# Performance work log

Hardware: AMD Instinct MI355X
Metric: run time of the kernel (lower is better)

## Reference

```python
import jax, jax.numpy as jnp
import numpy as np

N_NODES = 100000
N_EDGES = 1600000
IN_C, HID_C, OUT_C = 26, 128, 64
BN_EPS = 1e-5
WEIGHT_TABLE = jnp.array([0.7,0.9,0.7,0.9,0.3,0.7,0.3,0.9,0.3,0.3,0.9,0.7,0.1,
                          0.9,0.5,0.9,0.5,0.5,0.1,0.3,0.7,0.9,0.9,0.9,0.9,0.9],
                         dtype=jnp.float32)


def setup_inputs() -> dict:
    key = jax.random.key(0)
    ks = jax.random.split(key, 20)
    d = {}
    d['h'] = jax.random.normal(ks[0], (N_NODES, IN_C), dtype=jnp.float32)
    d['src'] = jax.random.randint(ks[1], (N_EDGES,), 0, N_NODES, dtype=jnp.int32)
    d['dst'] = jax.random.randint(ks[2], (N_EDGES,), 0, N_NODES, dtype=jnp.int32)
    # GraphConv weights (Glorot-ish scale)
    d['w0'] = jax.random.normal(ks[3], (IN_C, HID_C), dtype=jnp.float32) * (1.0 / np.sqrt(IN_C))
    d['b0'] = jnp.zeros((HID_C,), jnp.float32)
    d['w1'] = jax.random.normal(ks[4], (HID_C, HID_C), dtype=jnp.float32) * (1.0 / np.sqrt(HID_C))
    d['b1'] = jnp.zeros((HID_C,), jnp.float32)
    d['w2'] = jax.random.normal(ks[5], (HID_C, HID_C), dtype=jnp.float32) * (1.0 / np.sqrt(HID_C))
    d['b2'] = jnp.zeros((HID_C,), jnp.float32)
    # BatchNorm affine params
    for i in range(3):
        d[f'g{i}'] = jnp.ones((HID_C,), jnp.float32)
        d[f'bt{i}'] = jnp.zeros((HID_C,), jnp.float32)
    d['wfc'] = jax.random.normal(ks[6], (HID_C, OUT_C), dtype=jnp.float32) * (1.0 / np.sqrt(HID_C))
    d['bfc'] = jnp.zeros((OUT_C,), jnp.float32)
    return d


def _degree_norms(src, dst):
    ones = jnp.ones((N_EDGES,), jnp.float32)
    deg_out = jax.ops.segment_sum(ones, src, num_segments=N_NODES)
    deg_in = jax.ops.segment_sum(ones, dst, num_segments=N_NODES)
    norm_src = jnp.clip(deg_out, 1.0, None) ** -0.5  # [N]
    norm_dst = jnp.clip(deg_in, 1.0, None) ** -0.5   # [N]
    return norm_src[:, None], norm_dst[:, None]


def _graph_conv(h, W, b, src, dst, norm_src, norm_dst):
    # DGL GraphConv, norm='both': D_dst^{-1/2} A^T D_src^{-1/2} X W + b
    y = (h * norm_src) @ W                                   # [N, out]
    agg = jax.ops.segment_sum(y[src], dst, num_segments=N_NODES)
    return agg * norm_dst + b


def _batch_norm(x, gamma, beta):
    mu = jnp.mean(x, axis=0)
    var = jnp.mean((x - mu) ** 2, axis=0)
    return (x - mu) * jax.lax.rsqrt(var + BN_EPS) * gamma + beta


def reference(h, src, dst, w0, b0, w1, b1, w2, b2,
              g0, bt0, g1, bt1, g2, bt2, wfc, bfc):
    node_cats = jnp.argmax(h, axis=1)
    node_weights = WEIGHT_TABLE[node_cats][:, None]  # [N,1]
    norm_src, norm_dst = _degree_norms(src, dst)
    x = h
    for W, b, g, bt in ((w0, b0, g0, bt0), (w1, b1, g1, bt1), (w2, b2, g2, bt2)):
        x = _graph_conv(x, W, b, src, dst, norm_src, norm_dst)
        x = _batch_norm(x, g, bt)
        x = jax.nn.relu(x)
    out = x @ wfc + bfc
    return out, node_weights
```

## Files before the change

### kernel.cpp

```cpp
#include <hip/hip_runtime.h>

#define NN 100000
#define NE 1600000
#define BN_EPS 1e-5f
#define CSHIFT 9
#define NBC ((NN + 511) >> CSHIFT)
#define CAPC 10240
#define EPB1 4096
#define NBLK1 ((NE + EPB1 - 1)/EPB1)
#define NTILES ((NN + 63)/64)
#define GGRID 521
#define NPAGE 64

typedef short bf16x8 __attribute__((ext_vector_type(8)));
typedef float f32x4  __attribute__((ext_vector_type(4)));

__constant__ float c_wtab[26] = {0.7f,0.9f,0.7f,0.9f,0.3f,0.7f,0.3f,0.9f,0.3f,0.3f,0.9f,0.7f,0.1f,
                                 0.9f,0.5f,0.9f,0.5f,0.5f,0.1f,0.3f,0.7f,0.9f,0.9f,0.9f,0.9f,0.9f};

__device__ __forceinline__ unsigned f2bf(float f){
    unsigned u = __float_as_uint(f);
    return (u + 0x7fffu + ((u >> 16) & 1u)) >> 16;
}
__device__ __forceinline__ float bflo(unsigned v){ return __uint_as_float(v << 16); }
__device__ __forceinline__ float bfhi(unsigned v){ return __uint_as_float(v & 0xffff0000u); }

__global__ void k_prepw(const float* __restrict__ w0, const float* __restrict__ w1,
                        const float* __restrict__ w2, const float* __restrict__ wfc,
                        unsigned short* __restrict__ wt){
    int i = blockIdx.x*256 + threadIdx.x;
    if (i < 4096){
        int c = i >> 5, k = i & 31;
        float v = (k < 26) ? w0[k*128 + c] : 0.f;
        wt[i] = (unsigned short)f2bf(v);
    } else if (i < 20480){
        int j = i - 4096; int c = j >> 7, k = j & 127;
        wt[i] = (unsigned short)f2bf(w1[k*128 + c]);
    } else if (i < 36864){
        int j = i - 20480; int c = j >> 7, k = j & 127;
        wt[i] = (unsigned short)f2bf(w2[k*128 + c]);
    } else if (i < 45056){
        int j = i - 36864; int c = j >> 7, k = j & 127;
        wt[i] = (unsigned short)f2bf(wfc[k*64 + c]);
    }
}

__global__ void k_init(unsigned* __restrict__ gcurD, unsigned* __restrict__ gcurS){
    int i = blockIdx.x*256 + threadIdx.x;
    if (i < NBC){ gcurD[i] = (unsigned)i*CAPC; gcurS[i] = (unsigned)i*CAPC; }
}

__global__ __launch_bounds__(512) void k_radix1(const int* __restrict__ src,
                                                const int* __restrict__ dst,
                                                unsigned* __restrict__ gcurD,
                                                unsigned* __restrict__ gcurS,
                                                unsigned* __restrict__ pairs,
                                                unsigned short* __restrict__ tok){
    __shared__ unsigned hD[NBC], hS[NBC];
    int tid = threadIdx.x;
    for (int i = tid; i < NBC; i += 512){ hD[i] = 0u; hS[i] = 0u; }
    __syncthreads();
    int base = blockIdx.x*EPB1;
    int n = NE - base; if (n > EPB1) n = EPB1;
    for (int k = tid; k < n; k += 512){
        atomicAdd(&hD[(unsigned)dst[base+k] >> CSHIFT], 1u);
        atomicAdd(&hS[(unsigned)src[base+k] >> CSHIFT], 1u);
    }
    __syncthreads();
    for (int i = tid; i < NBC; i += 512){
        unsigned c = hD[i];
        hD[i] = c ? atomicAdd(&gcurD[i], c) : 0u;
        c = hS[i];
        hS[i] = c ? atomicAdd(&gcurS[i], c) : 0u;
    }
    __syncthreads();
    for (int k = tid; k < n; k += 512){
        int d = dst[base+k], s = src[base+k];
        unsigned bb = (unsigned)d >> CSHIFT;
        unsigned p = atomicAdd(&hD[bb], 1u);
        if (p < (bb+1)*CAPC)
            pairs[p] = ((unsigned)(d & 511) << 17) | (unsigned)s;
        bb = (unsigned)s >> CSHIFT;
        p = atomicAdd(&hS[bb], 1u);
        if (p < (bb+1)*CAPC)
            tok[p] = (unsigned short)(s & 511);
    }
}

__global__ __launch_bounds__(1024) void k_radix2(const unsigned* __restrict__ gcurD,
                                                 const unsigned* __restrict__ gcurS,
                                                 const unsigned* __restrict__ pairs,
                                                 const unsigned short* __restrict__ tok,
                                                 int* __restrict__ csr,
                                                 unsigned* __restrict__ offs,
                                                 unsigned* __restrict__ degi,
                                                 unsigned* __restrict__ dego){
    __shared__ unsigned cnt[512], cur[512], scnt[512];
    int b = blockIdx.x, tid = threadIdx.x;
    if (tid < 512){ cnt[tid] = 0u; scnt[tid] = 0u; }
    __syncthreads();
    unsigned baseC = (unsigned)b*CAPC;
    unsigned nD = gcurD[b] - baseC; if (nD > CAPC) nD = CAPC;
    unsigned nS = gcurS[b] - baseC; if (nS > CAPC) nS = CAPC;
    for (unsigned i = tid; i < nD; i += 1024)
        atomicAdd(&cnt[pairs[baseC + i] >> 17], 1u);
    for (unsigned i = tid; i < nS; i += 1024)
        atomicAdd(&scnt[tok[baseC + i]], 1u);
    __syncthreads();
    if (tid < 512) cur[tid] = cnt[tid];
    __syncthreads();
    for (int o = 1; o < 512; o <<= 1){
        unsigned x = 0;
        if (tid < 512 && tid >= o) x = cur[tid - o];
        __syncthreads();
        if (tid < 512) cur[tid] += x;
        __syncthreads();
    }
    if (tid < 512){
        unsigned ex = cur[tid] - cnt[tid];
        int node = (b << CSHIFT) + tid;
        if (node < NN){
            offs[node] = baseC + ex;
            degi[node] = cnt[tid];
            dego[node] = scnt[tid];
        }
        cur[tid] = ex;
    }
    __syncthreads();
    for (unsigned i = tid; i < nD; i += 1024){
        unsigned pr = pairs[baseC + i];
        unsigned p = atomicAdd(&cur[pr >> 17], 1u);
        csr[baseC + p] = (int)(pr & 0x1FFFFu);
    }
}

__global__ void k_node(const float* __restrict__ h, const unsigned* __restrict__ dego,
                       const unsigned* __restrict__ degi, float* __restrict__ nsrc,
                       float* __restrict__ ndst, float* __restrict__ outw,
                       unsigned* __restrict__ xn0){
    int i = blockIdx.x*blockDim.x + threadIdx.x;
    if (i < NN){
        float d0 = (float)dego[i]; d0 = d0 < 1.f ? 1.f : d0;
        float d1 = (float)degi[i]; d1 = d1 < 1.f ? 1.f : d1;
        float ns = rsqrtf(d0);
        nsrc[i] = ns;
        ndst[i] = rsqrtf(d1);
        float row[26];
        #pragma unroll
        for (int c = 0; c < 26; ++c) row[c] = h[(size_t)i*26 + c];
        float best = row[0]; int bi = 0;
        #pragma unroll
        for (int c = 1; c < 26; ++c){ if (row[c] > best){ best = row[c]; bi = c; } }
        outw[i] = c_wtab[bi];
        #pragma unroll
        for (int d = 0; d < 13; ++d)
            xn0[(size_t)i*16 + d] = f2bf(row[2*d]*ns) | (f2bf(row[2*d+1]*ns) << 16);
        #pragma unroll
        for (int d = 13; d < 16; ++d) xn0[(size_t)i*16 + d] = 0u;
    }
}

__global__ __launch_bounds__(64) void k_agg0(const uint4* __restrict__ xn,
                                             const unsigned* __restrict__ offs,
                                             const unsigned* __restrict__ degi,
                                             const int* __restrict__ csr,
                                             uint4* __restrict__ agg){
    int node = blockIdx.x;
    int lane = threadIdx.x;
    int g = lane >> 2, q = lane & 3;
    unsigned beg = offs[node], end = beg + degi[node];
    float a[8];
    #pragma unroll
    for (int j = 0; j < 8; ++j) a[j] = 0.f;
    for (unsigned e = beg + (unsigned)g; e < end; e += 16){
        uint4 v = xn[(size_t)csr[e]*4 + q];
        a[0] += bflo(v.x); a[1] += bfhi(v.x);
        a[2] += bflo(v.y); a[3] += bfhi(v.y);
        a[4] += bflo(v.z); a[5] += bfhi(v.z);
        a[6] += bflo(v.w); a[7] += bfhi(v.w);
    }
    #pragma unroll
    for (int j = 0; j < 8; ++j){
        a[j] += __shfl_xor(a[j], 4);
        a[j] += __shfl_xor(a[j], 8);
        a[j] += __shfl_xor(a[j], 16);
        a[j] += __shfl_xor(a[j], 32);
    }
    if (g == 0){
        uint4 o;
        o.x = f2bf(a[0]) | (f2bf(a[1]) << 16);
        o.y = f2bf(a[2]) | (f2bf(a[3]) << 16);
        o.z = f2bf(a[4]) | (f2bf(a[5]) << 16);
        o.w = f2bf(a[6]) | (f2bf(a[7]) << 16);
        agg[(size_t)node*4 + q] = o;
    }
}

__global__ __launch_bounds__(64) void k_agg_bf(const uint4* __restrict__ xn,
                                               const unsigned* __restrict__ offs,
                                               const unsigned* __restrict__ degi,
                                               const int* __restrict__ csr,
                                               uint4* __restrict__ agg){
    int node = blockIdx.x;
    int lane = threadIdx.x;
    int g = lane >> 4, q = lane & 15;
    unsigned beg = offs[node], end = beg + degi[node];
    float a[8];
    #pragma unroll
    for (int j = 0; j < 8; ++j) a[j] = 0.f;
    unsigned e = beg + (unsigned)g;
    for (; e + 12 < end; e += 16){
        int s0 = csr[e], s1 = csr[e+4], s2 = csr[e+8], s3 = csr[e+12];
        uint4 v0 = xn[(size_t)s0*16 + q];
        uint4 v1 = xn[(size_t)s1*16 + q];
        uint4 v2 = xn[(size_t)s2*16 + q];
        uint4 v3 = xn[(size_t)s3*16 + q];
        a[0] += bflo(v0.x) + bflo(v1.x) + bflo(v2.x) + bflo(v3.x);
        a[1] += bfhi(v0.x) + bfhi(v1.x) + bfhi(v2.x) + bfhi(v3.x);
        a[2] += bflo(v0.y) + bflo(v1.y) + bflo(v2.y) + bflo(v3.y);
        a[3] += bfhi(v0.y) + bfhi(v1.y) + bfhi(v2.y) + bfhi(v3.y);
        a[4] += bflo(v0.z) + bflo(v1.z) + bflo(v2.z) + bflo(v3.z);
        a[5] += bfhi(v0.z) + bfhi(v1.z) + bfhi(v2.z) + bfhi(v3.z);
        a[6] += bflo(v0.w) + bflo(v1.w) + bflo(v2.w) + bflo(v3.w);
        a[7] += bfhi(v0.w) + bfhi(v1.w) + bfhi(v2.w) + bfhi(v3.w);
    }
    for (; e < end; e += 4){
        uint4 v = xn[(size_t)csr[e]*16 + q];
        a[0] += bflo(v.x); a[1] += bfhi(v.x);
        a[2] += bflo(v.y); a[3] += bfhi(v.y);
        a[4] += bflo(v.z); a[5] += bfhi(v.z);
        a[6] += bflo(v.w); a[7] += bfhi(v.w);
    }
    #pragma unroll
    for (int j = 0; j < 8; ++j){
        a[j] += __shfl_xor(a[j], 16);
        a[j] += __shfl_xor(a[j], 32);
    }
    if (g == 0){
        uint4 o;
        o.x = f2bf(a[0]) | (f2bf(a[1]) << 16);
        o.y = f2bf(a[2]) | (f2bf(a[3]) << 16);
        o.z = f2bf(a[4]) | (f2bf(a[5]) << 16);
        o.w = f2bf(a[6]) | (f2bf(a[7]) << 16);
        agg[(size_t)node*16 + q] = o;
    }
}

template<int CIN, int COUT, bool STATS, bool NDST, bool F32OUT>
__global__ __launch_bounds__(256) void k_gemm_mfma(const unsigned short* __restrict__ A,
                                                   const unsigned short* __restrict__ Bt,
                                                   const float* __restrict__ bias,
                                                   const float* __restrict__ ndst,
                                                   void* __restrict__ Zv,
                                                   float* __restrict__ part){
    constexpr int KD4 = CIN/8;
    constexpr int NT = COUT/16;
    __shared__ char sA[64*CIN*2];
    __shared__ char sB[COUT*CIN*2];
    __shared__ float sS[2][COUT];
    float* Zf = (float*)Zv;
    unsigned short* Zh = (unsigned short*)Zv;
    const int tid = threadIdx.x;
    const int w = tid >> 6, lane = tid & 63;
    const int lrow = lane & 15, kg = lane >> 4;

    const uint4* B4 = (const uint4*)Bt;
    for (int i = tid; i < COUT*KD4; i += 256){
        int cc = i/KD4, c4 = i - cc*KD4;
        *(uint4*)(sB + ((cc*CIN*2 + c4*16) ^ ((cc&7)<<4))) = B4[i];
    }
    if (STATS){
        for (int i = tid; i < 2*COUT; i += 256) (&sS[0][0])[i] = 0.f;
    }

    float cs[NT], cq[NT];
    #pragma unroll
    for (int n = 0; n < NT; ++n){ cs[n] = 0.f; cq[n] = 0.f; }

    const uint4* A4 = (const uint4*)A;
    const uint4 z4 = make_uint4(0,0,0,0);
    for (int t = blockIdx.x; t < NTILES; t += GGRID){
        const int row0 = t*64;
        for (int i = tid; i < 64*KD4; i += 256){
            int r = i/KD4, c4 = i - r*KD4;
            int gr = row0 + r;
            uint4 v = (gr < NN) ? A4[(size_t)gr*KD4 + c4] : z4;
            *(uint4*)(sA + ((r*CIN*2 + c4*16) ^ ((r&7)<<4))) = v;
        }
        __syncthreads();
        f32x4 acc[NT];
        #pragma unroll
        for (int n = 0; n < NT; ++n) acc[n] = (f32x4){0.f,0.f,0.f,0.f};
        const int arow = w*16 + lrow;
        #pragma unroll
        for (int kk = 0; kk < CIN/32; ++kk){
            const int kb = kk*64 + kg*16;
            bf16x8 af = *(const bf16x8*)(sA + ((arow*CIN*2 + kb) ^ ((arow&7)<<4)));
            #pragma unroll
            for (int n = 0; n < NT; ++n){
                int bc = n*16 + lrow;
                bf16x8 bv = *(const bf16x8*)(sB + ((bc*CIN*2 + kb) ^ ((bc&7)<<4)));
                acc[n] = __builtin_amdgcn_mfma_f32_16x16x32_bf16(af, bv, acc[n], 0, 0, 0);
            }
        }
        int grow[4]; float nm[4]; bool val[4];
        #pragma unroll
        for (int j = 0; j < 4; ++j){
            grow[j] = row0 + w*16 + kg*4 + j;
            val[j]  = grow[j] < NN;
            nm[j]   = (NDST && val[j]) ? ndst[grow[j]] : 1.f;
        }
        #pragma unroll
        for (int n = 0; n < NT; ++n){
            int gcol = n*16 + lrow;
            float bv = bias[gcol];
            #pragma unroll
            for (int j = 0; j < 4; ++j){
                float z = acc[n][j]*nm[j] + bv;
                if (val[j]){
                    if (F32OUT) Zf[(size_t)grow[j]*COUT + gcol] = z;
                    else        Zh[(size_t)grow[j]*COUT + gcol] = (unsigned short)f2bf(z);
                    if (STATS){ cs[n] += z; cq[n] += z*z; }
                }
            }
        }
        __syncthreads();
    }
    if (STATS){
        #pragma unroll
        for (int n = 0; n < NT; ++n){
            float s = cs[n], q = cq[n];
            s += __shfl_xor(s, 16); s += __shfl_xor(s, 32);
            q += __shfl_xor(q, 16); q += __shfl_xor(q, 32);
            if (kg == 0){
                atomicAdd(&sS[0][n*16 + lrow], s);
                atomicAdd(&sS[1][n*16 + lrow], q);
            }
        }
        __syncthreads();
        float* pg = part + (size_t)(blockIdx.x & (NPAGE-1))*2*COUT;
        for (int i = tid; i < 2*COUT; i += 256)
            atomicAdd(&pg[i], (&sS[0][0])[i]);
    }
}

__global__ void k_bnfin(const float* __restrict__ part, float* __restrict__ stats,
                        const float* __restrict__ g, const float* __restrict__ bt){
    int c = threadIdx.x;
    float s = 0.f, q = 0.f;
    #pragma unroll 8
    for (int p = 0; p < NPAGE; ++p){
        s += part[p*256 + c];
        q += part[p*256 + 128 + c];
    }
    float mu  = s / (float)NN;
    float var = q / (float)NN - mu*mu;
    if (var < 0.f) var = 0.f;
    float sc = g[c] * rsqrtf(var + BN_EPS);
    stats[256 + c] = sc;
    stats[384 + c] = bt[c] - mu*sc;
}

__global__ void k_bnapply_bf(const unsigned* __restrict__ Xb, const float* __restrict__ stats,
                             const float* __restrict__ nsrc, unsigned* __restrict__ out){
    int idx = blockIdx.x*blockDim.x + threadIdx.x;
    if (idx < NN*64){
        int d = idx & 63;
        int node = idx >> 6;
        int c0 = d << 1;
        unsigned v = Xb[idx];
        float v0 = bflo(v)*stats[256 + c0]     + stats[384 + c0];
        float v1 = bfhi(v)*stats[256 + c0 + 1] + stats[384 + c0 + 1];
        float ns = nsrc ? nsrc[node] : 1.f;
        v0 = v0 > 0.f ? v0*ns : 0.f;
        v1 = v1 > 0.f ? v1*ns : 0.f;
        out[idx] = f2bf(v0) | (f2bf(v1) << 16);
    }
}

extern "C" void kernel_launch(void* const* d_in, const int* in_sizes, int n_in,
                              void* d_out, int out_size, void* d_ws, size_t ws_size,
                              hipStream_t stream) {
    const float* h   = (const float*)d_in[0];
    const int*   src = (const int*)d_in[1];
    const int*   dst = (const int*)d_in[2];
    const float* w0  = (const float*)d_in[3];
    const float* b0  = (const float*)d_in[4];
    const float* w1  = (const float*)d_in[5];
    const float* b1  = (const float*)d_in[6];
    const float* w2  = (const float*)d_in[7];
    const float* b2  = (const float*)d_in[8];
    const float* g0  = (const float*)d_in[9];
    const float* bt0 = (const float*)d_in[10];
    const float* g1  = (const float*)d_in[11];
    const float* bt1 = (const float*)d_in[12];
    const float* g2  = (const float*)d_in[13];
    const float* bt2 = (const float*)d_in[14];
    const float* wfc = (const float*)d_in[15];
    const float* bfc = (const float*)d_in[16];

    float* out   = (float*)d_out;
    float* out_w = out + (size_t)NN*64;

    char* ws = (char*)d_ws;
    size_t off = 0;
    auto alloc = [&](size_t b){ size_t p = off; off += (b + 255) & ~(size_t)255; return ws + p; };

    unsigned*       dego    = (unsigned*)alloc((size_t)NN*4);
    unsigned*       degi    = (unsigned*)alloc((size_t)NN*4);
    float*          nsrc    = (float*)   alloc((size_t)NN*4);
    float*          ndst    = (float*)   alloc((size_t)NN*4);
    unsigned*       offsets = (unsigned*)alloc((size_t)NN*4);
    unsigned*       gcurD   = (unsigned*)alloc((size_t)NBC*4);
    unsigned*       gcurS   = (unsigned*)alloc((size_t)NBC*4);
    float*          stats   = (float*)   alloc(3*512*4);
    float*          spart   = (float*)   alloc(3*(size_t)NPAGE*256*4);
    unsigned short* wt      = (unsigned short*)alloc(45056*2);
    int*            csr     = (int*)     alloc((size_t)NBC*CAPC*4);
    unsigned*       xn0     = (unsigned*)alloc((size_t)NN*16*4);
    unsigned short* bufA    = (unsigned short*)alloc((size_t)NN*128*2);
    float*          bufB    = (float*)   alloc((size_t)NN*128*4);
    unsigned*       bufC    = (unsigned*)alloc((size_t)NN*64*4);
    (void)ws_size; (void)in_sizes; (void)n_in; (void)out_size;

    unsigned*       pairs = (unsigned*)bufB;
    unsigned short* tok   = (unsigned short*)((char*)bufB + (size_t)NBC*CAPC*4);
    uint4*          aggB  = (uint4*)bufB;

    hipMemsetAsync(spart, 0, 3*(size_t)NPAGE*256*4, stream);

    k_prepw<<<176, 256, 0, stream>>>(w0, w1, w2, wfc, wt);
    k_init<<<1, 256, 0, stream>>>(gcurD, gcurS);
    k_radix1<<<NBLK1, 512, 0, stream>>>(src, dst, gcurD, gcurS, pairs, tok);
    k_radix2<<<NBC, 1024, 0, stream>>>(gcurD, gcurS, pairs, tok, csr, offsets, degi, dego);
    k_node<<<(NN + 255)/256, 256, 0, stream>>>(h, dego, degi, nsrc, ndst, out_w, xn0);

    k_agg0<<<NN, 64, 0, stream>>>((const uint4*)xn0, offsets, degi, csr, aggB);
    k_gemm_mfma<32,128,true,true,false><<<GGRID, 256, 0, stream>>>((const unsigned short*)aggB, wt, b0,
                                                                   ndst, bufA, spart + 0*NPAGE*256);
    k_bnfin<<<1, 128, 0, stream>>>(spart + 0*NPAGE*256, stats + 0*512, g0, bt0);
    k_bnapply_bf<<<(NN*64 + 255)/256, 256, 0, stream>>>((unsigned*)bufA, stats + 0*512, nsrc, bufC);

    k_agg_bf<<<NN, 64, 0, stream>>>((const uint4*)bufC, offsets, degi, csr, aggB);
    k_gemm_mfma<128,128,true,true,false><<<GGRID, 256, 0, stream>>>((const unsigned short*)aggB, wt + 4096,
                                                                    b1, ndst, bufA, spart + 1*NPAGE*256);
    k_bnfin<<<1, 128, 0, stream>>>(spart + 1*NPAGE*256, stats + 1*512, g1, bt1);
    k_bnapply_bf<<<(NN*64 + 255)/256, 256, 0, stream>>>((unsigned*)bufA, stats + 1*512, nsrc, bufC);

    k_agg_bf<<<NN, 64, 0, stream>>>((const uint4*)bufC, offsets, degi, csr, aggB);
    k_gemm_mfma<128,128,true,true,false><<<GGRID, 256, 0, stream>>>((const unsigned short*)aggB, wt + 20480,
                                                                    b2, ndst, bufA, spart + 2*NPAGE*256);
    k_bnfin<<<1, 128, 0, stream>>>(spart + 2*NPAGE*256, stats + 2*512, g2, bt2);
    k_bnapply_bf<<<(NN*64 + 255)/256, 256, 0, stream>>>((unsigned*)bufA, stats + 2*512, nullptr, bufC);

    k_gemm_mfma<128,64,false,false,true><<<GGRID, 256, 0, stream>>>((unsigned short*)bufC, wt + 36864, bfc,
                                                                    nullptr, out, nullptr);
}
```

Before: 370.5 us.

## Store hidden features in 16-channel slices and aggregate per slice

Node features are now stored as 8 slices of 16 channels each, so one slice holds 32 bytes per node. The aggregation kernel gives each block one slice for 8 nodes, and each pair of lanes gathers one edge's 32-byte fragment. BN-apply writes this sliced layout and the GEMMs read it through a new SLICED template flag. The aim is a smaller working set per gather for better cache locality, at the cost of 8x more reads of the CSR index and smaller, less coalesced memory transactions per edge.

```diff
diff --git a/kernel.cpp b/kernel.cpp
--- a/kernel.cpp
+++ b/kernel.cpp
@@ -11,6 +11,7 @@
 #define NTILES ((NN + 63)/64)
 #define GGRID 521
 #define NPAGE 64
+#define SLNN ((size_t)NN*2)
 
 typedef short bf16x8 __attribute__((ext_vector_type(8)));
 typedef float f32x4  __attribute__((ext_vector_type(4)));
@@ -196,36 +197,27 @@
     }
 }
 
-__global__ __launch_bounds__(64) void k_agg_bf(const uint4* __restrict__ xn,
-                                               const unsigned* __restrict__ offs,
-                                               const unsigned* __restrict__ degi,
-                                               const int* __restrict__ csr,
-                                               uint4* __restrict__ agg){
-    int node = blockIdx.x;
-    int lane = threadIdx.x;
-    int g = lane >> 4, q = lane & 15;
+__global__ __launch_bounds__(256) void k_agg_bf(const uint4* __restrict__ xnS,
+                                                const unsigned* __restrict__ offs,
+                                                const unsigned* __restrict__ degi,
+                                                const int* __restrict__ csr,
+                                                uint4* __restrict__ aggS){
+    const int slice = blockIdx.x & 7;
+    const int ng = blockIdx.x >> 3;
+    const int tid = threadIdx.x;
+    const int w = tid >> 6, lane = tid & 63;
+    const int half = lane >> 5;
+    const int node = ng*8 + w*2 + half;
+    const int el = (lane & 31) >> 1;
+    const int q = lane & 1;
+    const uint4* base = xnS + (size_t)slice*SLNN;
     unsigned beg = offs[node], end = beg + degi[node];
     float a[8];
     #pragma unroll
     for (int j = 0; j < 8; ++j) a[j] = 0.f;
-    unsigned e = beg + (unsigned)g;
-    for (; e + 12 < end; e += 16){
-        int s0 = csr[e], s1 = csr[e+4], s2 = csr[e+8], s3 = csr[e+12];
-        uint4 v0 = xn[(size_t)s0*16 + q];
-        uint4 v1 = xn[(size_t)s1*16 + q];
-        uint4 v2 = xn[(size_t)s2*16 + q];
-        uint4 v3 = xn[(size_t)s3*16 + q];
-        a[0] += bflo(v0.x) + bflo(v1.x) + bflo(v2.x) + bflo(v3.x);
-        a[1] += bfhi(v0.x) + bfhi(v1.x) + bfhi(v2.x) + bfhi(v3.x);
-        a[2] += bflo(v0.y) + bflo(v1.y) + bflo(v2.y) + bflo(v3.y);
-        a[3] += bfhi(v0.y) + bfhi(v1.y) + bfhi(v2.y) + bfhi(v3.y);
-        a[4] += bflo(v0.z) + bflo(v1.z) + bflo(v2.z) + bflo(v3.z);
-        a[5] += bfhi(v0.z) + bfhi(v1.z) + bfhi(v2.z) + bfhi(v3.z);
-        a[6] += bflo(v0.w) + bflo(v1.w) + bflo(v2.w) + bflo(v3.w);
-        a[7] += bfhi(v0.w) + bfhi(v1.w) + bfhi(v2.w) + bfhi(v3.w);
-    }
-    for (; e < end; e += 4){
-        uint4 v = xn[(size_t)csr[e]*16 + q];
+    for (unsigned e = beg + (unsigned)el; e < end; e += 16){
+        int s = csr[e];
+        uint4 v = base[(size_t)s*2 + q];
         a[0] += bflo(v.x); a[1] += bfhi(v.x);
         a[2] += bflo(v.y); a[3] += bfhi(v.y);
         a[4] += bflo(v.z); a[5] += bfhi(v.z);
@@ -233,20 +225,22 @@
     }
     #pragma unroll
     for (int j = 0; j < 8; ++j){
+        a[j] += __shfl_xor(a[j], 2);
+        a[j] += __shfl_xor(a[j], 4);
+        a[j] += __shfl_xor(a[j], 8);
         a[j] += __shfl_xor(a[j], 16);
-        a[j] += __shfl_xor(a[j], 32);
-    }
-    if (g == 0){
+    }
+    if (el == 0){
         uint4 o;
         o.x = f2bf(a[0]) | (f2bf(a[1]) << 16);
         o.y = f2bf(a[2]) | (f2bf(a[3]) << 16);
         o.z = f2bf(a[4]) | (f2bf(a[5]) << 16);
         o.w = f2bf(a[6]) | (f2bf(a[7]) << 16);
-        agg[(size_t)node*16 + q] = o;
-    }
-}
-
-template<int CIN, int COUT, bool STATS, bool NDST, bool F32OUT>
+        aggS[(size_t)slice*SLNN + (size_t)node*2 + q] = o;
+    }
+}
+
+template<int CIN, int COUT, bool STATS, bool NDST, bool F32OUT, bool SLICED>
 __global__ __launch_bounds__(256) void k_gemm_mfma(const unsigned short* __restrict__ A,
                                                    const unsigned short* __restrict__ Bt,
                                                    const float* __restrict__ bias,
@@ -284,7 +278,11 @@
         for (int i = tid; i < 64*KD4; i += 256){
             int r = i/KD4, c4 = i - r*KD4;
             int gr = row0 + r;
-            uint4 v = (gr < NN) ? A4[(size_t)gr*KD4 + c4] : z4;
+            uint4 v;
+            if (gr < NN){
+                if (SLICED) v = A4[(size_t)(c4 >> 1)*SLNN + (size_t)gr*2 + (c4 & 1)];
+                else        v = A4[(size_t)gr*KD4 + c4];
+            } else v = z4;
             *(uint4*)(sA + ((r*CIN*2 + c4*16) ^ ((r&7)<<4))) = v;
         }
         __syncthreads();
@@ -362,7 +360,7 @@
 }
 
 __global__ void k_bnapply_bf(const unsigned* __restrict__ Xb, const float* __restrict__ stats,
-                             const float* __restrict__ nsrc, unsigned* __restrict__ out){
+                             const float* __restrict__ nsrc, unsigned* __restrict__ outS){
     int idx = blockIdx.x*blockDim.x + threadIdx.x;
     if (idx < NN*64){
         int d = idx & 63;
@@ -374,7 +372,8 @@
         float ns = nsrc ? nsrc[node] : 1.f;
         v0 = v0 > 0.f ? v0*ns : 0.f;
         v1 = v1 > 0.f ? v1*ns : 0.f;
-        out[idx] = f2bf(v0) | (f2bf(v1) << 16);
+        int slice = d >> 3, dd = d & 7;
+        outS[(size_t)slice*NN*8 + (size_t)node*8 + dd] = f2bf(v0) | (f2bf(v1) << 16);
     }
 }
 
@@ -436,23 +435,23 @@
     k_node<<<(NN + 255)/256, 256, 0, stream>>>(h, dego, degi, nsrc, ndst, out_w, xn0);
 
     k_agg0<<<NN, 64, 0, stream>>>((const uint4*)xn0, offsets, degi, csr, aggB);
-    k_gemm_mfma<32,128,true,true,false><<<GGRID, 256, 0, stream>>>((const unsigned short*)aggB, wt, b0,
-                                                                   ndst, bufA, spart + 0*NPAGE*256);
+    k_gemm_mfma<32,128,true,true,false,false><<<GGRID, 256, 0, stream>>>((const unsigned short*)aggB, wt, b0,
+                                                                         ndst, bufA, spart + 0*NPAGE*256);
     k_bnfin<<<1, 128, 0, stream>>>(spart + 0*NPAGE*256, stats + 0*512, g0, bt0);
     k_bnapply_bf<<<(NN*64 + 255)/256, 256, 0, stream>>>((unsigned*)bufA, stats + 0*512, nsrc, bufC);
 
-    k_agg_bf<<<NN, 64, 0, stream>>>((const uint4*)bufC, offsets, degi, csr, aggB);
-    k_gemm_mfma<128,128,true,true,false><<<GGRID, 256, 0, stream>>>((const unsigned short*)aggB, wt + 4096,
-                                                                    b1, ndst, bufA, spart + 1*NPAGE*256);
+    k_agg_bf<<<NN, 256, 0, stream>>>((const uint4*)bufC, offsets, degi, csr, aggB);
+    k_gemm_mfma<128,128,true,true,false,true><<<GGRID, 256, 0, stream>>>((const unsigned short*)aggB, wt + 4096,
+                                                                         b1, ndst, bufA, spart + 1*NPAGE*256);
     k_bnfin<<<1, 128, 0, stream>>>(spart + 1*NPAGE*256, stats + 1*512, g1, bt1);
     k_bnapply_bf<<<(NN*64 + 255)/256, 256, 0, stream>>>((unsigned*)bufA, stats + 1*512, nsrc, bufC);
 
-    k_agg_bf<<<NN, 64, 0, stream>>>((const uint4*)bufC, offsets, degi, csr, aggB);
-    k_gemm_mfma<128,128,true,true,false><<<GGRID, 256, 0, stream>>>((const unsigned short*)aggB, wt + 20480,
-                                                                    b2, ndst, bufA, spart + 2*NPAGE*256);
+    k_agg_bf<<<NN, 256, 0, stream>>>((const uint4*)bufC, offsets, degi, csr, aggB);
+    k_gemm_mfma<128,128,true,true,false,true><<<GGRID, 256, 0, stream>>>((const unsigned short*)aggB, wt + 20480,
+                                                                         b2, ndst, bufA, spart + 2*NPAGE*256);
     k_bnfin<<<1, 128, 0, stream>>>(spart + 2*NPAGE*256, stats + 2*512, g2, bt2);
     k_bnapply_bf<<<(NN*64 + 255)/256, 256, 0, stream>>>((unsigned*)bufA, stats + 2*512, nullptr, bufC);
 
-    k_gemm_mfma<128,64,false,false,true><<<GGRID, 256, 0, stream>>>((unsigned short*)bufC, wt + 36864, bfc,
-                                                                    nullptr, out, nullptr);
-}
+    k_gemm_mfma<128,64,false,false,true,true><<<GGRID, 256, 0, stream>>>((unsigned short*)bufC, wt + 36864, bfc,
+                                                                         nullptr, out, nullptr);
+}
```

Measured after the change: 523.9 us. 41.4% more time.

## Fuse BN-apply/ReLU into aggregation and final GEMM; merge prep and node kernels

Applied to the files above, without the earlier changes.

Removes the three standalone BatchNorm-apply kernels. The scale/shift, ReLU and source-norm are now applied on the fly inside the gather-aggregation (per edge) and inside the final GEMM's A-tile load. Folds k_init into weight prep and the per-node norm/argmax kernel into radix2, which cuts launches and the dego buffer. Each gathered row now costs extra FMAs plus a per-edge nsrc load, trading compute for one fewer full read/write pass per layer.

```diff
diff --git a/kernel.cpp b/kernel.cpp
--- a/kernel.cpp
+++ b/kernel.cpp
@@ -25,9 +25,10 @@
 __device__ __forceinline__ float bflo(unsigned v){ return __uint_as_float(v << 16); }
 __device__ __forceinline__ float bfhi(unsigned v){ return __uint_as_float(v & 0xffff0000u); }
 
-__global__ void k_prepw(const float* __restrict__ w0, const float* __restrict__ w1,
-                        const float* __restrict__ w2, const float* __restrict__ wfc,
-                        unsigned short* __restrict__ wt){
+__global__ void k_prep(const float* __restrict__ w0, const float* __restrict__ w1,
+                       const float* __restrict__ w2, const float* __restrict__ wfc,
+                       unsigned short* __restrict__ wt,
+                       unsigned* __restrict__ gcurD, unsigned* __restrict__ gcurS){
     int i = blockIdx.x*256 + threadIdx.x;
     if (i < 4096){
         int c = i >> 5, k = i & 31;
@@ -43,10 +44,6 @@
         int j = i - 36864; int c = j >> 7, k = j & 127;
         wt[i] = (unsigned short)f2bf(wfc[k*64 + c]);
     }
-}
-
-__global__ void k_init(unsigned* __restrict__ gcurD, unsigned* __restrict__ gcurS){
-    int i = blockIdx.x*256 + threadIdx.x;
     if (i < NBC){ gcurD[i] = (unsigned)i*CAPC; gcurS[i] = (unsigned)i*CAPC; }
 }
 
@@ -87,14 +84,18 @@
     }
 }
 
-__global__ __launch_bounds__(1024) void k_radix2(const unsigned* __restrict__ gcurD,
-                                                 const unsigned* __restrict__ gcurS,
-                                                 const unsigned* __restrict__ pairs,
-                                                 const unsigned short* __restrict__ tok,
-                                                 int* __restrict__ csr,
-                                                 unsigned* __restrict__ offs,
-                                                 unsigned* __restrict__ degi,
-                                                 unsigned* __restrict__ dego){
+__global__ __launch_bounds__(1024) void k_radix2n(const unsigned* __restrict__ gcurD,
+                                                  const unsigned* __restrict__ gcurS,
+                                                  const unsigned* __restrict__ pairs,
+                                                  const unsigned short* __restrict__ tok,
+                                                  const float* __restrict__ h,
+                                                  int* __restrict__ csr,
+                                                  unsigned* __restrict__ offs,
+                                                  unsigned* __restrict__ degi,
+                                                  float* __restrict__ nsrc,
+                                                  float* __restrict__ ndst,
+                                                  float* __restrict__ outw,
+                                                  unsigned* __restrict__ xn0){
     __shared__ unsigned cnt[512], cur[512], scnt[512];
     int b = blockIdx.x, tid = threadIdx.x;
     if (tid < 512){ cnt[tid] = 0u; scnt[tid] = 0u; }
@@ -122,7 +123,6 @@
         if (node < NN){
             offs[node] = baseC + ex;
             degi[node] = cnt[tid];
-            dego[node] = scnt[tid];
         }
         cur[tid] = ex;
     }
@@ -132,31 +132,27 @@
         unsigned p = atomicAdd(&cur[pr >> 17], 1u);
         csr[baseC + p] = (int)(pr & 0x1FFFFu);
     }
-}
-
-__global__ void k_node(const float* __restrict__ h, const unsigned* __restrict__ dego,
-                       const unsigned* __restrict__ degi, float* __restrict__ nsrc,
-                       float* __restrict__ ndst, float* __restrict__ outw,
-                       unsigned* __restrict__ xn0){
-    int i = blockIdx.x*blockDim.x + threadIdx.x;
-    if (i < NN){
-        float d0 = (float)dego[i]; d0 = d0 < 1.f ? 1.f : d0;
-        float d1 = (float)degi[i]; d1 = d1 < 1.f ? 1.f : d1;
-        float ns = rsqrtf(d0);
-        nsrc[i] = ns;
-        ndst[i] = rsqrtf(d1);
-        float row[26];
-        #pragma unroll
-        for (int c = 0; c < 26; ++c) row[c] = h[(size_t)i*26 + c];
-        float best = row[0]; int bi = 0;
-        #pragma unroll
-        for (int c = 1; c < 26; ++c){ if (row[c] > best){ best = row[c]; bi = c; } }
-        outw[i] = c_wtab[bi];
-        #pragma unroll
-        for (int d = 0; d < 13; ++d)
-            xn0[(size_t)i*16 + d] = f2bf(row[2*d]*ns) | (f2bf(row[2*d+1]*ns) << 16);
-        #pragma unroll
-        for (int d = 13; d < 16; ++d) xn0[(size_t)i*16 + d] = 0u;
+    if (tid < 512){
+        int node = (b << CSHIFT) + tid;
+        if (node < NN){
+            float d0 = (float)scnt[tid]; d0 = d0 < 1.f ? 1.f : d0;
+            float d1 = (float)cnt[tid];  d1 = d1 < 1.f ? 1.f : d1;
+            float ns = rsqrtf(d0);
+            nsrc[node] = ns;
+            ndst[node] = rsqrtf(d1);
+            float row[26];
+            #pragma unroll
+            for (int c = 0; c < 26; ++c) row[c] = h[(size_t)node*26 + c];
+            float best = row[0]; int bi = 0;
+            #pragma unroll
+            for (int c = 1; c < 26; ++c){ if (row[c] > best){ best = row[c]; bi = c; } }
+            outw[node] = c_wtab[bi];
+            #pragma unroll
+            for (int d = 0; d < 13; ++d)
+                xn0[(size_t)node*16 + d] = f2bf(row[2*d]*ns) | (f2bf(row[2*d+1]*ns) << 16);
+            #pragma unroll
+            for (int d = 13; d < 16; ++d) xn0[(size_t)node*16 + d] = 0u;
+        }
     }
 }
 
@@ -196,7 +192,9 @@
     }
 }
 
-__global__ __launch_bounds__(64) void k_agg_bf(const uint4* __restrict__ xn,
+__global__ __launch_bounds__(64) void k_agg_bn(const uint4* __restrict__ zt,
+                                               const float* __restrict__ st,
+                                               const float* __restrict__ nsrc,
                                                const unsigned* __restrict__ offs,
                                                const unsigned* __restrict__ degi,
                                                const int* __restrict__ csr,
@@ -204,6 +202,12 @@
     int node = blockIdx.x;
     int lane = threadIdx.x;
     int g = lane >> 4, q = lane & 15;
+    float sc8[8], sh8[8];
+    #pragma unroll
+    for (int j = 0; j < 8; ++j){
+        sc8[j] = st[256 + q*8 + j];
+        sh8[j] = st[384 + q*8 + j];
+    }
     unsigned beg = offs[node], end = beg + degi[node];
     float a[8];
     #pragma unroll
@@ -211,25 +215,39 @@
     unsigned e = beg + (unsigned)g;
     for (; e + 12 < end; e += 16){
         int s0 = csr[e], s1 = csr[e+4], s2 = csr[e+8], s3 = csr[e+12];
-        uint4 v0 = xn[(size_t)s0*16 + q];
-        uint4 v1 = xn[(size_t)s1*16 + q];
-        uint4 v2 = xn[(size_t)s2*16 + q];
-        uint4 v3 = xn[(size_t)s3*16 + q];
-        a[0] += bflo(v0.x) + bflo(v1.x) + bflo(v2.x) + bflo(v3.x);
-        a[1] += bfhi(v0.x) + bfhi(v1.x) + bfhi(v2.x) + bfhi(v3.x);
-        a[2] += bflo(v0.y) + bflo(v1.y) + bflo(v2.y) + bflo(v3.y);
-        a[3] += bfhi(v0.y) + bfhi(v1.y) + bfhi(v2.y) + bfhi(v3.y);
-        a[4] += bflo(v0.z) + bflo(v1.z) + bflo(v2.z) + bflo(v3.z);
-        a[5] += bfhi(v0.z) + bfhi(v1.z) + bfhi(v2.z) + bfhi(v3.z);
-        a[6] += bflo(v0.w) + bflo(v1.w) + bflo(v2.w) + bflo(v3.w);
-        a[7] += bfhi(v0.w) + bfhi(v1.w) + bfhi(v2.w) + bfhi(v3.w);
+        float n0 = nsrc[s0], n1 = nsrc[s1], n2 = nsrc[s2], n3 = nsrc[s3];
+        uint4 v0 = zt[(size_t)s0*16 + q];
+        uint4 v1 = zt[(size_t)s1*16 + q];
+        uint4 v2 = zt[(size_t)s2*16 + q];
+        uint4 v3 = zt[(size_t)s3*16 + q];
+        #pragma unroll
+        for (int k = 0; k < 4; ++k){
+            uint4 v = (k==0)?v0:(k==1)?v1:(k==2)?v2:v3;
+            float nn = (k==0)?n0:(k==1)?n1:(k==2)?n2:n3;
+            float t;
+            t = fmaf(bflo(v.x), sc8[0], sh8[0]); t = t > 0.f ? t : 0.f; a[0] = fmaf(t, nn, a[0]);
+            t = fmaf(bfhi(v.x), sc8[1], sh8[1]); t = t > 0.f ? t : 0.f; a[1] = fmaf(t, nn, a[1]);
+            t = fmaf(bflo(v.y), sc8[2], sh8[2]); t = t > 0.f ? t : 0.f; a[2] = fmaf(t, nn, a[2]);
+            t = fmaf(bfhi(v.y), sc8[3], sh8[3]); t = t > 0.f ? t : 0.f; a[3] = fmaf(t, nn, a[3]);
+            t = fmaf(bflo(v.z), sc8[4], sh8[4]); t = t > 0.f ? t : 0.f; a[4] = fmaf(t, nn, a[4]);
+            t = fmaf(bfhi(v.z), sc8[5], sh8[5]); t = t > 0.f ? t : 0.f; a[5] = fmaf(t, nn, a[5]);
+            t = fmaf(bflo(v.w), sc8[6], sh8[6]); t = t > 0.f ? t : 0.f; a[6] = fmaf(t, nn, a[6]);
+            t = fmaf(bfhi(v.w), sc8[7], sh8[7]); t = t > 0.f ? t : 0.f; a[7] = fmaf(t, nn, a[7]);
+        }
     }
     for (; e < end; e += 4){
-        uint4 v = xn[(size_t)csr[e]*16 + q];
-        a[0] += bflo(v.x); a[1] += bfhi(v.x);
-        a[2] += bflo(v.y); a[3] += bfhi(v.y);
-        a[4] += bflo(v.z); a[5] += bfhi(v.z);
-        a[6] += bflo(v.w); a[7] += bfhi(v.w);
+        int s = csr[e];
+        float nn = nsrc[s];
+        uint4 v = zt[(size_t)s*16 + q];
+        float t;
+        t = fmaf(bflo(v.x), sc8[0], sh8[0]); t = t > 0.f ? t : 0.f; a[0] = fmaf(t, nn, a[0]);
+        t = fmaf(bfhi(v.x), sc8[1], sh8[1]); t = t > 0.f ? t : 0.f; a[1] = fmaf(t, nn, a[1]);
+        t = fmaf(bflo(v.y), sc8[2], sh8[2]); t = t > 0.f ? t : 0.f; a[2] = fmaf(t, nn, a[2]);
+        t = fmaf(bfhi(v.y), sc8[3], sh8[3]); t = t > 0.f ? t : 0.f; a[3] = fmaf(t, nn, a[3]);
+        t = fmaf(bflo(v.z), sc8[4], sh8[4]); t = t > 0.f ? t : 0.f; a[4] = fmaf(t, nn, a[4]);
+        t = fmaf(bfhi(v.z), sc8[5], sh8[5]); t = t > 0.f ? t : 0.f; a[5] = fmaf(t, nn, a[5]);
+        t = fmaf(bflo(v.w), sc8[6], sh8[6]); t = t > 0.f ? t : 0.f; a[6] = fmaf(t, nn, a[6]);
+        t = fmaf(bfhi(v.w), sc8[7], sh8[7]); t = t > 0.f ? t : 0.f; a[7] = fmaf(t, nn, a[7]);
     }
     #pragma unroll
     for (int j = 0; j < 8; ++j){
@@ -246,13 +264,14 @@
     }
 }
 
-template<int CIN, int COUT, bool STATS, bool NDST, bool F32OUT>
+template<int CIN, int COUT, bool STATS, bool NDST, bool F32OUT, bool BNIN>
 __global__ __launch_bounds__(256) void k_gemm_mfma(const unsigned short* __restrict__ A,
                                                    const unsigned short* __restrict__ Bt,
                                                    const float* __restrict__ bias,
                                                    const float* __restrict__ ndst,
                                                    void* __restrict__ Zv,
-                                                   float* __restrict__ part){
+                                                   float* __restrict__ part,
+                                                   const float* __restrict__ bn){
     constexpr int KD4 = CIN/8;
     constexpr int NT = COUT/16;
     __shared__ char sA[64*CIN*2];
@@ -285,6 +304,19 @@
             int r = i/KD4, c4 = i - r*KD4;
             int gr = row0 + r;
             uint4 v = (gr < NN) ? A4[(size_t)gr*KD4 + c4] : z4;
+            if (BNIN && gr < NN){
+                int ch = c4*8;
+                unsigned dw[4] = {v.x, v.y, v.z, v.w};
+                #pragma unroll
+                for (int k = 0; k < 4; ++k){
+                    float f0 = fmaf(bflo(dw[k]), bn[256 + ch + 2*k],     bn[384 + ch + 2*k]);
+                    float f1 = fmaf(bfhi(dw[k]), bn[256 + ch + 2*k + 1], bn[384 + ch + 2*k + 1]);
+                    f0 = f0 > 0.f ? f0 : 0.f;
+                    f1 = f1 > 0.f ? f1 : 0.f;
+                    dw[k] = f2bf(f0) | (f2bf(f1) << 16);
+                }
+                v = make_uint4(dw[0], dw[1], dw[2], dw[3]);
+            }
             *(uint4*)(sA + ((r*CIN*2 + c4*16) ^ ((r&7)<<4))) = v;
         }
         __syncthreads();
@@ -359,23 +391,6 @@
     float sc = g[c] * rsqrtf(var + BN_EPS);
     stats[256 + c] = sc;
     stats[384 + c] = bt[c] - mu*sc;
-}
-
-__global__ void k_bnapply_bf(const unsigned* __restrict__ Xb, const float* __restrict__ stats,
-                             const float* __restrict__ nsrc, unsigned* __restrict__ out){
-    int idx = blockIdx.x*blockDim.x + threadIdx.x;
-    if (idx < NN*64){
-        int d = idx & 63;
-        int node = idx >> 6;
-        int c0 = d << 1;
-        unsigned v = Xb[idx];
-        float v0 = bflo(v)*stats[256 + c0]     + stats[384 + c0];
-        float v1 = bfhi(v)*stats[256 + c0 + 1] + stats[384 + c0 + 1];
-        float ns = nsrc ? nsrc[node] : 1.f;
-        v0 = v0 > 0.f ? v0*ns : 0.f;
-        v1 = v1 > 0.f ? v1*ns : 0.f;
-        out[idx] = f2bf(v0) | (f2bf(v1) << 16);
-    }
 }
 
 extern "C" void kernel_launch(void* const* d_in, const int* in_sizes, int n_in,
@@ -406,7 +421,6 @@
     size_t off = 0;
     auto alloc = [&](size_t b){ size_t p = off; off += (b + 255) & ~(size_t)255; return ws + p; };
 
-    unsigned*       dego    = (unsigned*)alloc((size_t)NN*4);
     unsigned*       degi    = (unsigned*)alloc((size_t)NN*4);
     float*          nsrc    = (float*)   alloc((size_t)NN*4);
     float*          ndst    = (float*)   alloc((size_t)NN*4);
@@ -420,7 +434,6 @@
     unsigned*       xn0     = (unsigned*)alloc((size_t)NN*16*4);
     unsigned short* bufA    = (unsigned short*)alloc((size_t)NN*128*2);
     float*          bufB    = (float*)   alloc((size_t)NN*128*4);
-    unsigned*       bufC    = (unsigned*)alloc((size_t)NN*64*4);
     (void)ws_size; (void)in_sizes; (void)n_in; (void)out_size;
 
     unsigned*       pairs = (unsigned*)bufB;
@@ -429,30 +442,28 @@
 
     hipMemsetAsync(spart, 0, 3*(size_t)NPAGE*256*4, stream);
 
-    k_prepw<<<176, 256, 0, stream>>>(w0, w1, w2, wfc, wt);
-    k_init<<<1, 256, 0, stream>>>(gcurD, gcurS);
+    k_prep<<<176, 256, 0, stream>>>(w0, w1, w2, wfc, wt, gcurD, gcurS);
     k_radix1<<<NBLK1, 512, 0, stream>>>(src, dst, gcurD, gcurS, pairs, tok);
-    k_radix2<<<NBC, 1024, 0, stream>>>(gcurD, gcurS, pairs, tok, csr, offsets, degi, dego);
-    k_node<<<(NN + 255)/256, 256, 0, stream>>>(h, dego, degi, nsrc, ndst, out_w, xn0);
+    k_radix2n<<<NBC, 1024, 0, stream>>>(gcurD, gcurS, pairs, tok, h, csr, offsets, degi,
+                                        nsrc, ndst, out_w, xn0);
 
     k_agg0<<<NN, 64, 0, stream>>>((const uint4*)xn0, offsets, degi, csr, aggB);
-    k_gemm_mfma<32,128,true,true,false><<<GGRID, 256, 0, stream>>>((const unsigned short*)aggB, wt, b0,
-                                                                   ndst, bufA, spart + 0*NPAGE*256);
+    k_gemm_mfma<32,128,true,true,false,false><<<GGRID, 256, 0, stream>>>(
+        (const unsigned short*)aggB, wt, b0, ndst, bufA, spart + 0*NPAGE*256, nullptr);
     k_bnfin<<<1, 128, 0, stream>>>(spart + 0*NPAGE*256, stats + 0*512, g0, bt0);
-    k_bnapply_bf<<<(NN*64 + 255)/256, 256, 0, stream>>>((unsigned*)bufA, stats + 0*512, nsrc, bufC);
-
-    k_agg_bf<<<NN, 64, 0, stream>>>((const uint4*)bufC, offsets, degi, csr, aggB);
-    k_gemm_mfma<128,128,true,true,false><<<GGRID, 256, 0, stream>>>((const unsigned short*)aggB, wt + 4096,
-                                                                    b1, ndst, bufA, spart + 1*NPAGE*256);
+
+    k_agg_bn<<<NN, 64, 0, stream>>>((const uint4*)bufA, stats + 0*512, nsrc,
+                                    offsets, degi, csr, aggB);
+    k_gemm_mfma<128,128,true,true,false,false><<<GGRID, 256, 0, stream>>>(
+        (const unsigned short*)aggB, wt + 4096, b1, ndst, bufA, spart + 1*NPAGE*256, nullptr);
     k_bnfin<<<1, 128, 0, stream>>>(spart + 1*NPAGE*256, stats + 1*512, g1, bt1);
-    k_bnapply_bf<<<(NN*64 + 255)/256, 256, 0, stream>>>((unsigned*)bufA, stats + 1*512, nsrc, bufC);
-
-    k_agg_bf<<<NN, 64, 0, stream>>>((const uint4*)bufC, offsets, degi, csr, aggB);
-    k_gemm_mfma<128,128,true,true,false><<<GGRID, 256, 0, stream>>>((const unsigned short*)aggB, wt + 20480,
-                                                                    b2, ndst, bufA, spart + 2*NPAGE*256);
+
+    k_agg_bn<<<NN, 64, 0, stream>>>((const uint4*)bufA, stats + 1*512, nsrc,
+                                    offsets, degi, csr, aggB);
+    k_gemm_mfma<128,128,true,true,false,false><<<GGRID, 256, 0, stream>>>(
+        (const unsigned short*)aggB, wt + 20480, b2, ndst, bufA, spart + 2*NPAGE*256, nullptr);
     k_bnfin<<<1, 128, 0, stream>>>(spart + 2*NPAGE*256, stats + 2*512, g2, bt2);
-    k_bnapply_bf<<<(NN*64 + 255)/256, 256, 0, stream>>>((unsigned*)bufA, stats + 2*512, nullptr, bufC);
-
-    k_gemm_mfma<128,64,false,false,true><<<GGRID, 256, 0, stream>>>((unsigned short*)bufC, wt + 36864, bfc,
-                                                                    nullptr, out, nullptr);
-}
+
+    k_gemm_mfma<128,64,false,false,true,true><<<GGRID, 256, 0, stream>>>(
+        bufA, wt + 36864, bfc, nullptr, out, nullptr, stats + 2*512);
+}
```

Result: faster. 337.5 us (-8.9%).
